# Kernel optimization log

Measured on AMD Instinct MI355X. Metric: run time of the kernel, lower is better.

Reference implementation:

```python
import jax, jax.numpy as jnp
import numpy as np


def setup_inputs() -> dict:
    key = jax.random.key(0)
    k1, k2, k3 = jax.random.split(key, 3)
    N, C, W = 32, 64, 4096
    F, WW = 128, 64
    x = jax.random.normal(k1, (N, C, W), dtype=jnp.float32)
    w = jax.random.normal(k2, (F, C, WW), dtype=jnp.float32)
    b = jax.random.normal(k3, (F,), dtype=jnp.float32)
    return {"x": x, "w": w, "b": b}


def reference(x, w, b):
    # FFT-based 1D cross-correlation (the original loops over N, F, C; here batched).
    # x: [N, C, W], w: [F, C, WW], b: [F]
    N, C, W = x.shape
    F, _, WW = w.shape
    pad = 0  # module's padding kwarg
    fftsize = 1 << int(np.ceil(np.log2(W + 2 * pad + WW - 1)))  # next_power2
    out_W = W + 2 * pad - WW + 1
    # rfft of zero-padded signals and filters
    xfft = jnp.fft.rfft(x, n=fftsize, axis=-1)          # [N, C, K]
    wfft = jnp.fft.rfft(w, n=fftsize, axis=-1)          # [F, C, K]
    # cross-correlation: multiply by conj of filter spectrum, sum over channels
    offt = jnp.einsum('nck,fck->nfk', xfft, jnp.conj(wfft))  # [N, F, K]
    out = jnp.fft.irfft(offt, n=fftsize, axis=-1)[..., :out_W]  # real part, first out_W samples
    return out + b[None, :, None]
```

## Files before the change

kernel.cpp:

```cpp
#include <hip/hip_runtime.h>


#define C_TOT   64
#define F_TOT   128
#define KW      64
#define OUT_W   4033
#define W_IN    4096
#define N_BATCH 32
#define T_BLK   256
#define XROW    4352
#define CH      2

typedef __attribute__((ext_vector_type(8))) short  short8;
typedef __attribute__((ext_vector_type(4))) float  floatx4;

union Frag { unsigned int u[4]; short8 v; };

__device__ inline unsigned short f32_to_bf16(float f) {
  unsigned int u = __float_as_uint(f);
  u += 0x7FFF + ((u >> 16) & 1);
  return (unsigned short)(u >> 16);
}

__device__ inline void async16(const unsigned short* g, unsigned short* l) {
  __builtin_amdgcn_global_load_lds(
      (const __attribute__((address_space(1))) unsigned int*)g,
      (__attribute__((address_space(3))) unsigned int*)l, 16, 0, 0);
}

__global__ __launch_bounds__(256) void conv1d_prep(
    const float* __restrict__ x, const float* __restrict__ w,
    unsigned short* __restrict__ xb, unsigned short* __restrict__ wsw) {
  int bid = blockIdx.x;
  if (bid < N_BATCH * C_TOT) {
    const float* src = x + (size_t)bid * W_IN;
    unsigned short* dst = xb + (size_t)bid * XROW;
    for (int i = threadIdx.x; i < XROW / 4; i += 256) {
      int t = i * 4;
      ushort4 o;
      if (t < W_IN) {
        float4 v = *(const float4*)(src + t);
        o.x = f32_to_bf16(v.x); o.y = f32_to_bf16(v.y);
        o.z = f32_to_bf16(v.z); o.w = f32_to_bf16(v.w);
      } else {
        o.x = o.y = o.z = o.w = 0;
      }
      *(ushort4*)(dst + t) = o;
    }
  } else {
    int i4 = (bid - N_BATCH * C_TOT) * 256 + threadIdx.x;
    if (i4 < F_TOT * C_TOT * KW / 4) {
      int k4 = (i4 & 15) * 4;
      int c  = (i4 >> 4) & 63;
      int f  = i4 >> 10;
      float4 v = *(const float4*)&w[(size_t)i4 * 4];
      ushort4 o;
      o.x = f32_to_bf16(v.x); o.y = f32_to_bf16(v.y);
      o.z = f32_to_bf16(v.z); o.w = f32_to_bf16(v.w);
      int chunk = (k4 >> 3) ^ (f & 7);
      *(ushort4*)&wsw[((size_t)(c * F_TOT + f) * 8 + chunk) * 8 + (k4 & 7)] = o;
    }
  }
}

__global__ __launch_bounds__(256, 2) void conv1d_mfma(
    const unsigned short* __restrict__ xb, const unsigned short* __restrict__ wsw,
    const float* __restrict__ b, float* __restrict__ out) {
  __shared__ union SM {
    unsigned short wls[2][CH * F_TOT * KW];
    float tr[32 * 256];
  } sm;

  const int tid  = threadIdx.x;
  const int lane = tid & 63;
  const int wv   = tid >> 6;
  const int q    = lane >> 4;
  const int col  = lane & 15;
  const int n    = blockIdx.y;
  const int t0   = blockIdx.x * T_BLK;
  const int fh2  = wv & 1;
  const int th   = wv >> 1;

  floatx4 acc[8][4];
#pragma unroll
  for (int ms = 0; ms < 8; ++ms)
#pragma unroll
    for (int ft = 0; ft < 4; ++ft) acc[ms][ft] = (floatx4)0.0f;

  const unsigned short* xrowb = xb + (size_t)(n * C_TOT) * XROW + t0
                              + 8 * col + 128 * th + 8 * q;

#define STAGE_W(cg, p)                                                          \
  {                                                                             \
    const unsigned short* wbase = wsw + (size_t)(cg) * (CH * F_TOT * KW);       \
    _Pragma("unroll")                                                           \
    for (int s = 0; s < 8; ++s) {                                               \
      int off = (wv * 8 + s) * 512;                                             \
      async16(wbase + off + lane * 8, &sm.wls[p][off]);                         \
    }                                                                           \
  }

  STAGE_W(0, 0)
  __syncthreads();

  for (int cg = 0; cg < C_TOT / CH; ++cg) {
    const int p = cg & 1;
    if (cg < C_TOT / CH - 1) STAGE_W(cg + 1, p ^ 1)

#pragma unroll
    for (int chl = 0; chl < CH; ++chl) {
      const unsigned short* xpb = xrowb + (size_t)(cg * CH + chl) * XROW;
      const unsigned short* wpb = &sm.wls[p][chl * F_TOT * KW];
#pragma unroll
      for (int h = 0; h < 2; ++h) {
        const uint4 d0 = *(const uint4*)(xpb + 32 * h);
        const uint4 d1 = *(const uint4*)(xpb + 32 * h + 8);
        const unsigned int D[8] = {d0.x, d0.y, d0.z, d0.w, d1.x, d1.y, d1.z, d1.w};
        Frag A[8];
#pragma unroll
        for (int s = 0; s < 4; ++s)
#pragma unroll
          for (int i = 0; i < 4; ++i) {
            A[2 * s].u[i]     = D[s + i];
            A[2 * s + 1].u[i] = (D[s + i] >> 16) | (D[s + i + 1] << 16);
          }
        const int bs = ((h * 4 + q) ^ (col & 7)) * 8;
#pragma unroll
        for (int ft = 0; ft < 4; ++ft) {
          const short8 bf =
              *(const short8*)&wpb[(fh2 * 64 + ft * 16 + col) * KW + bs];
#pragma unroll
          for (int ms = 0; ms < 8; ++ms)
            acc[ms][ft] =
                __builtin_amdgcn_mfma_f32_16x16x32_bf16(A[ms].v, bf, acc[ms][ft], 0, 0, 0);
        }
      }
    }
    __syncthreads();
  }

  const int fs_w  = fh2 * 16 + col;
  const int fs_r  = tid >> 3;
  const int seg   = tid & 7;
  const int f_r   = (fs_r >> 4) * 64 + (fs_r & 15);
  const size_t ob = ((size_t)n * F_TOT) * OUT_W;

#pragma unroll
  for (int j = 0; j < 4; ++j) {
#pragma unroll
    for (int r = 0; r < 4; ++r)
#pragma unroll
      for (int g = 0; g < 2; ++g) {
        float4 vv;
        vv.x = acc[g * 4 + 0][j][r];
        vv.y = acc[g * 4 + 1][j][r];
        vv.z = acc[g * 4 + 2][j][r];
        vv.w = acc[g * 4 + 3][j][r];
        int chunk = 8 * q + 2 * r + g + 32 * th;
        *(float4*)&sm.tr[fs_w * 256 + ((chunk ^ (fs_w & 7)) << 2)] = vv;
      }
    __syncthreads();
    const int f = f_r + 16 * j;
    const float bias = b[f];
    const size_t obf = ob + (size_t)f * OUT_W;
#pragma unroll
    for (int j2 = 0; j2 < 8; ++j2) {
      int chunk = seg + 8 * j2;
      float4 vv = *(const float4*)&sm.tr[fs_r * 256 + ((chunk ^ (fs_r & 7)) << 2)];
      vv.x += bias; vv.y += bias; vv.z += bias; vv.w += bias;
      int t = t0 + chunk * 4;
      if (t + 3 < OUT_W) {
        *(float4*)&out[obf + t] = vv;
      } else {
        float e[4] = {vv.x, vv.y, vv.z, vv.w};
#pragma unroll
        for (int u = 0; u < 4; ++u)
          if (t + u < OUT_W) out[obf + t + u] = e[u];
      }
    }
    __syncthreads();
  }
}

extern "C" void kernel_launch(void* const* d_in, const int* in_sizes, int n_in,
                              void* d_out, int out_size, void* d_ws, size_t ws_size,
                              hipStream_t stream) {
  const float* x = (const float*)d_in[0];
  const float* w = (const float*)d_in[1];
  const float* b = (const float*)d_in[2];
  float* out = (float*)d_out;

  unsigned short* wsw = (unsigned short*)d_ws;
  unsigned short* xb  = (unsigned short*)((char*)d_ws + (1 << 20));

  conv1d_prep<<<N_BATCH * C_TOT + 512, 256, 0, stream>>>(x, w, xb, wsw);

  dim3 grid((OUT_W + T_BLK - 1) / T_BLK, N_BATCH);
  conv1d_mfma<<<grid, 256, 0, stream>>>(xb, wsw, b, out);
}
```

Baseline: 196.8 us.

## Load filter fragments directly from global into registers with double-buffered prefetch

Drops the LDS staging of weights through async global-to-LDS copies and the per-channel-group barriers. Each wave now reads its B fragments straight from global or L2 into registers, using a plain [c][f][k] bf16 layout, and double-buffers both A and B registers across channels. This removes the LDS traffic and sync overhead from the main loop. In exchange each wave issues more global loads, weight reuse across waves in a block relies on cache, and register pressure rises, which could hurt occupancy at two blocks per CU.

Measured after the change: 254.8 us. 1.29x slower.

```diff
diff --git a/kernel.cpp b/kernel.cpp
--- a/kernel.cpp
+++ b/kernel.cpp
@@ -9,7 +9,6 @@
 #define N_BATCH 32
 #define T_BLK   256
 #define XROW    4352
-#define CH      2
 
 typedef __attribute__((ext_vector_type(8))) short  short8;
 typedef __attribute__((ext_vector_type(4))) float  floatx4;
@@ -22,15 +21,9 @@
   return (unsigned short)(u >> 16);
 }
 
-__device__ inline void async16(const unsigned short* g, unsigned short* l) {
-  __builtin_amdgcn_global_load_lds(
-      (const __attribute__((address_space(1))) unsigned int*)g,
-      (__attribute__((address_space(3))) unsigned int*)l, 16, 0, 0);
-}
-
 __global__ __launch_bounds__(256) void conv1d_prep(
     const float* __restrict__ x, const float* __restrict__ w,
-    unsigned short* __restrict__ xb, unsigned short* __restrict__ wsw) {
+    unsigned short* __restrict__ xb, unsigned short* __restrict__ wcf) {
   int bid = blockIdx.x;
   if (bid < N_BATCH * C_TOT) {
     const float* src = x + (size_t)bid * W_IN;
@@ -57,19 +50,15 @@
       ushort4 o;
       o.x = f32_to_bf16(v.x); o.y = f32_to_bf16(v.y);
       o.z = f32_to_bf16(v.z); o.w = f32_to_bf16(v.w);
-      int chunk = (k4 >> 3) ^ (f & 7);
-      *(ushort4*)&wsw[((size_t)(c * F_TOT + f) * 8 + chunk) * 8 + (k4 & 7)] = o;
+      *(ushort4*)&wcf[((size_t)c * F_TOT + f) * KW + k4] = o;
     }
   }
 }
 
 __global__ __launch_bounds__(256, 2) void conv1d_mfma(
-    const unsigned short* __restrict__ xb, const unsigned short* __restrict__ wsw,
+    const unsigned short* __restrict__ xb, const unsigned short* __restrict__ wcf,
     const float* __restrict__ b, float* __restrict__ out) {
-  __shared__ union SM {
-    unsigned short wls[2][CH * F_TOT * KW];
-    float tr[32 * 256];
-  } sm;
+  __shared__ float tr[32 * 256];
 
   const int tid  = threadIdx.x;
   const int lane = tid & 63;
@@ -89,54 +78,60 @@
 
   const unsigned short* xrowb = xb + (size_t)(n * C_TOT) * XROW + t0
                               + 8 * col + 128 * th + 8 * q;
+  const unsigned short* wB = wcf + (size_t)(fh2 * 64 + col) * KW + 8 * q;
 
-#define STAGE_W(cg, p)                                                          \
+#define LOADB(B, c)                                                             \
   {                                                                             \
-    const unsigned short* wbase = wsw + (size_t)(cg) * (CH * F_TOT * KW);       \
+    const unsigned short* wp = wB + (size_t)(c) * (F_TOT * KW);                 \
     _Pragma("unroll")                                                           \
-    for (int s = 0; s < 8; ++s) {                                               \
-      int off = (wv * 8 + s) * 512;                                             \
-      async16(wbase + off + lane * 8, &sm.wls[p][off]);                         \
+    for (int ft = 0; ft < 4; ++ft) {                                            \
+      B[0][ft] = *(const short8*)(wp + ft * 16 * KW);                           \
+      B[1][ft] = *(const short8*)(wp + ft * 16 * KW + 32);                      \
     }                                                                           \
   }
 
-  STAGE_W(0, 0)
-  __syncthreads();
+#define LOADA(A, c)                                                             \
+  {                                                                             \
+    const unsigned short* xp = xrowb + (size_t)(c) * XROW;                      \
+    A[0] = *(const uint4*)(xp);      A[1] = *(const uint4*)(xp + 8);            \
+    A[2] = *(const uint4*)(xp + 32); A[3] = *(const uint4*)(xp + 40);           \
+  }
 
-  for (int cg = 0; cg < C_TOT / CH; ++cg) {
-    const int p = cg & 1;
-    if (cg < C_TOT / CH - 1) STAGE_W(cg + 1, p ^ 1)
+#define COMPUTE(Ax, Bx)                                                         \
+  {                                                                             \
+    _Pragma("unroll")                                                           \
+    for (int h = 0; h < 2; ++h) {                                               \
+      const unsigned int D[8] = {Ax[2 * h].x, Ax[2 * h].y, Ax[2 * h].z,         \
+                                 Ax[2 * h].w, Ax[2 * h + 1].x, Ax[2 * h + 1].y, \
+                                 Ax[2 * h + 1].z, Ax[2 * h + 1].w};             \
+      Frag F8[8];                                                               \
+      _Pragma("unroll")                                                         \
+      for (int s = 0; s < 4; ++s)                                               \
+        _Pragma("unroll")                                                       \
+        for (int i = 0; i < 4; ++i) {                                           \
+          F8[2 * s].u[i]     = D[s + i];                                        \
+          F8[2 * s + 1].u[i] = (D[s + i] >> 16) | (D[s + i + 1] << 16);         \
+        }                                                                       \
+      _Pragma("unroll")                                                         \
+      for (int ft = 0; ft < 4; ++ft)                                            \
+        _Pragma("unroll")                                                       \
+        for (int ms = 0; ms < 8; ++ms)                                          \
+          acc[ms][ft] = __builtin_amdgcn_mfma_f32_16x16x32_bf16(                \
+              F8[ms].v, Bx[h][ft], acc[ms][ft], 0, 0, 0);                       \
+    }                                                                           \
+  }
 
-#pragma unroll
-    for (int chl = 0; chl < CH; ++chl) {
-      const unsigned short* xpb = xrowb + (size_t)(cg * CH + chl) * XROW;
-      const unsigned short* wpb = &sm.wls[p][chl * F_TOT * KW];
-#pragma unroll
-      for (int h = 0; h < 2; ++h) {
-        const uint4 d0 = *(const uint4*)(xpb + 32 * h);
-        const uint4 d1 = *(const uint4*)(xpb + 32 * h + 8);
-        const unsigned int D[8] = {d0.x, d0.y, d0.z, d0.w, d1.x, d1.y, d1.z, d1.w};
-        Frag A[8];
-#pragma unroll
-        for (int s = 0; s < 4; ++s)
-#pragma unroll
-          for (int i = 0; i < 4; ++i) {
-            A[2 * s].u[i]     = D[s + i];
-            A[2 * s + 1].u[i] = (D[s + i] >> 16) | (D[s + i + 1] << 16);
-          }
-        const int bs = ((h * 4 + q) ^ (col & 7)) * 8;
-#pragma unroll
-        for (int ft = 0; ft < 4; ++ft) {
-          const short8 bf =
-              *(const short8*)&wpb[(fh2 * 64 + ft * 16 + col) * KW + bs];
-#pragma unroll
-          for (int ms = 0; ms < 8; ++ms)
-            acc[ms][ft] =
-                __builtin_amdgcn_mfma_f32_16x16x32_bf16(A[ms].v, bf, acc[ms][ft], 0, 0, 0);
-        }
-      }
-    }
-    __syncthreads();
+  uint4  A0[4], A1[4];
+  short8 B0[2][4], B1[2][4];
+  LOADA(A0, 0)
+  LOADB(B0, 0)
+#pragma unroll 1
+  for (int c = 0; c < C_TOT; c += 2) {
+    LOADA(A1, c + 1)
+    LOADB(B1, c + 1)
+    COMPUTE(A0, B0)
+    if (c + 2 < C_TOT) { LOADA(A0, c + 2) LOADB(B0, c + 2) }
+    COMPUTE(A1, B1)
   }
 
   const int fs_w  = fh2 * 16 + col;
@@ -145,6 +140,7 @@
   const int f_r   = (fs_r >> 4) * 64 + (fs_r & 15);
   const size_t ob = ((size_t)n * F_TOT) * OUT_W;
 
+  __syncthreads();
 #pragma unroll
   for (int j = 0; j < 4; ++j) {
 #pragma unroll
@@ -157,7 +153,7 @@
         vv.z = acc[g * 4 + 2][j][r];
         vv.w = acc[g * 4 + 3][j][r];
         int chunk = 8 * q + 2 * r + g + 32 * th;
-        *(float4*)&sm.tr[fs_w * 256 + ((chunk ^ (fs_w & 7)) << 2)] = vv;
+        *(float4*)&tr[fs_w * 256 + ((chunk ^ (fs_w & 7)) << 2)] = vv;
       }
     __syncthreads();
     const int f = f_r + 16 * j;
@@ -166,7 +162,7 @@
 #pragma unroll
     for (int j2 = 0; j2 < 8; ++j2) {
       int chunk = seg + 8 * j2;
-      float4 vv = *(const float4*)&sm.tr[fs_r * 256 + ((chunk ^ (fs_r & 7)) << 2)];
+      float4 vv = *(const float4*)&tr[fs_r * 256 + ((chunk ^ (fs_r & 7)) << 2)];
       vv.x += bias; vv.y += bias; vv.z += bias; vv.w += bias;
       int t = t0 + chunk * 4;
       if (t + 3 < OUT_W) {
@@ -190,11 +186,11 @@
   const float* b = (const float*)d_in[2];
   float* out = (float*)d_out;
 
-  unsigned short* wsw = (unsigned short*)d_ws;
+  unsigned short* wcf = (unsigned short*)d_ws;
   unsigned short* xb  = (unsigned short*)((char*)d_ws + (1 << 20));
 
-  conv1d_prep<<<N_BATCH * C_TOT + 512, 256, 0, stream>>>(x, w, xb, wsw);
+  conv1d_prep<<<N_BATCH * C_TOT + 512, 256, 0, stream>>>(x, w, xb, wcf);
 
   dim3 grid((OUT_W + T_BLK - 1) / T_BLK, N_BATCH);
-  conv1d_mfma<<<grid, 256, 0, stream>>>(xb, wsw, b, out);
+  conv1d_mfma<<<grid, 256, 0, stream>>>(xb, wcf, b, out);
 }
```

## Fuse input bf16 conversion into conv kernel and split filters across grid z

Applied to the files above, without the earlier changes.

Drops the separate x-to-bf16 prep pass: the MFMA kernel now reads fp32 x directly and packs it to bf16 in registers, with clamped indices standing in for the old zero-padded rows. Filters are split into two halves over a new grid z dimension, which halves the accumulators and LDS weight buffer per block and raises the launch-bounds occupancy target to 3. This removes a full read-write pass over x, but each block now loads twice as many input bytes per MFMA, and x is reloaded by both filter halves.

Result: slower. 273.3 us (+38.9%).

```diff
diff --git a/kernel.cpp b/kernel.cpp
--- a/kernel.cpp
+++ b/kernel.cpp
@@ -1,4 +1,5 @@
 #include <hip/hip_runtime.h>
+#include <hip/hip_bf16.h>
 
 
 #define C_TOT   64
@@ -8,7 +9,6 @@
 #define W_IN    4096
 #define N_BATCH 32
 #define T_BLK   256
-#define XROW    4352
 #define CH      2
 
 typedef __attribute__((ext_vector_type(8))) short  short8;
@@ -22,6 +22,11 @@
   return (unsigned short)(u >> 16);
 }
 
+__device__ inline unsigned int pack2(float a, float bb) {
+  __hip_bfloat162 h = __float22bfloat162_rn(make_float2(a, bb));
+  return *(unsigned int*)&h;
+}
+
 __device__ inline void async16(const unsigned short* g, unsigned short* l) {
   __builtin_amdgcn_global_load_lds(
       (const __attribute__((address_space(1))) unsigned int*)g,
@@ -29,45 +34,27 @@
 }
 
 __global__ __launch_bounds__(256) void conv1d_prep(
-    const float* __restrict__ x, const float* __restrict__ w,
-    unsigned short* __restrict__ xb, unsigned short* __restrict__ wsw) {
-  int bid = blockIdx.x;
-  if (bid < N_BATCH * C_TOT) {
-    const float* src = x + (size_t)bid * W_IN;
-    unsigned short* dst = xb + (size_t)bid * XROW;
-    for (int i = threadIdx.x; i < XROW / 4; i += 256) {
-      int t = i * 4;
-      ushort4 o;
-      if (t < W_IN) {
-        float4 v = *(const float4*)(src + t);
-        o.x = f32_to_bf16(v.x); o.y = f32_to_bf16(v.y);
-        o.z = f32_to_bf16(v.z); o.w = f32_to_bf16(v.w);
-      } else {
-        o.x = o.y = o.z = o.w = 0;
-      }
-      *(ushort4*)(dst + t) = o;
-    }
-  } else {
-    int i4 = (bid - N_BATCH * C_TOT) * 256 + threadIdx.x;
-    if (i4 < F_TOT * C_TOT * KW / 4) {
-      int k4 = (i4 & 15) * 4;
-      int c  = (i4 >> 4) & 63;
-      int f  = i4 >> 10;
-      float4 v = *(const float4*)&w[(size_t)i4 * 4];
-      ushort4 o;
-      o.x = f32_to_bf16(v.x); o.y = f32_to_bf16(v.y);
-      o.z = f32_to_bf16(v.z); o.w = f32_to_bf16(v.w);
-      int chunk = (k4 >> 3) ^ (f & 7);
-      *(ushort4*)&wsw[((size_t)(c * F_TOT + f) * 8 + chunk) * 8 + (k4 & 7)] = o;
-    }
-  }
-}
-
-__global__ __launch_bounds__(256, 2) void conv1d_mfma(
-    const unsigned short* __restrict__ xb, const unsigned short* __restrict__ wsw,
+    const float* __restrict__ w, unsigned short* __restrict__ wsw) {
+  int i4 = blockIdx.x * 256 + threadIdx.x;
+  if (i4 < F_TOT * C_TOT * KW / 4) {
+    int k4 = (i4 & 15) * 4;
+    int c  = (i4 >> 4) & 63;
+    int f  = i4 >> 10;
+    float4 v = *(const float4*)&w[(size_t)i4 * 4];
+    ushort4 o;
+    o.x = f32_to_bf16(v.x); o.y = f32_to_bf16(v.y);
+    o.z = f32_to_bf16(v.z); o.w = f32_to_bf16(v.w);
+    int fh = f >> 6, fl = f & 63;
+    int chunk = (k4 >> 3) ^ (f & 7);
+    *(ushort4*)&wsw[((size_t)((c * 2 + fh) * 64 + fl)) * 64 + chunk * 8 + (k4 & 7)] = o;
+  }
+}
+
+__global__ __launch_bounds__(256, 3) void conv1d_mfma(
+    const float* __restrict__ x, const unsigned short* __restrict__ wsw,
     const float* __restrict__ b, float* __restrict__ out) {
   __shared__ union SM {
-    unsigned short wls[2][CH * F_TOT * KW];
+    unsigned short wls[2][CH * 64 * KW];
     float tr[32 * 256];
   } sm;
 
@@ -78,89 +65,103 @@
   const int col  = lane & 15;
   const int n    = blockIdx.y;
   const int t0   = blockIdx.x * T_BLK;
-  const int fh2  = wv & 1;
+  const int fh   = blockIdx.z;
   const int th   = wv >> 1;
-
-  floatx4 acc[8][4];
+  const int fq   = wv & 1;
+
+  floatx4 acc[8][2];
 #pragma unroll
   for (int ms = 0; ms < 8; ++ms)
 #pragma unroll
-    for (int ft = 0; ft < 4; ++ft) acc[ms][ft] = (floatx4)0.0f;
-
-  const unsigned short* xrowb = xb + (size_t)(n * C_TOT) * XROW + t0
-                              + 8 * col + 128 * th + 8 * q;
+    for (int ft = 0; ft < 2; ++ft) acc[ms][ft] = (floatx4)0.0f;
+
+  const int tb = t0 + 8 * col + 128 * th + 8 * q;
+  const float* xnb = x + (size_t)n * C_TOT * W_IN;
 
 #define STAGE_W(cg, p)                                                          \
   {                                                                             \
-    const unsigned short* wbase = wsw + (size_t)(cg) * (CH * F_TOT * KW);       \
     _Pragma("unroll")                                                           \
-    for (int s = 0; s < 8; ++s) {                                               \
-      int off = (wv * 8 + s) * 512;                                             \
-      async16(wbase + off + lane * 8, &sm.wls[p][off]);                         \
+    for (int s = 0; s < 4; ++s) {                                               \
+      int g   = s * 256 + tid;                                                  \
+      int chl = g >> 9;                                                         \
+      int wo  = (g & 511) * 8;                                                  \
+      async16(wsw + ((size_t)(((cg) * CH + chl) * 2 + fh)) * 4096 + wo,         \
+              &sm.wls[p][g * 8]);                                               \
+    }                                                                           \
+  }
+
+#define COMPUTE(p)                                                              \
+  {                                                                             \
+    _Pragma("unroll")                                                           \
+    for (int chl = 0; chl < CH; ++chl) {                                        \
+      const float* xr = xnb + (size_t)(cg * CH + chl) * W_IN;                   \
+      const unsigned short* wpb = &sm.wls[p][chl * 4096];                       \
+      _Pragma("unroll")                                                         \
+      for (int h = 0; h < 2; ++h) {                                             \
+        const int gt = tb + 32 * h;                                             \
+        float4 v0 = *(const float4*)(xr + min(gt,      W_IN - 4));              \
+        float4 v1 = *(const float4*)(xr + min(gt + 4,  W_IN - 4));              \
+        float4 v2 = *(const float4*)(xr + min(gt + 8,  W_IN - 4));              \
+        float4 v3 = *(const float4*)(xr + min(gt + 12, W_IN - 4));              \
+        const unsigned int D[8] = {                                             \
+            pack2(v0.x, v0.y), pack2(v0.z, v0.w),                               \
+            pack2(v1.x, v1.y), pack2(v1.z, v1.w),                               \
+            pack2(v2.x, v2.y), pack2(v2.z, v2.w),                               \
+            pack2(v3.x, v3.y), pack2(v3.z, v3.w)};                              \
+        Frag A[8];                                                              \
+        _Pragma("unroll")                                                       \
+        for (int s = 0; s < 4; ++s)                                             \
+          _Pragma("unroll")                                                     \
+          for (int i = 0; i < 4; ++i) {                                         \
+            A[2 * s].u[i]     = D[s + i];                                       \
+            A[2 * s + 1].u[i] = (D[s + i] >> 16) | (D[s + i + 1] << 16);        \
+          }                                                                     \
+        const int bs = ((h * 4 + q) ^ (col & 7)) * 8;                           \
+        _Pragma("unroll")                                                       \
+        for (int ft = 0; ft < 2; ++ft) {                                        \
+          const short8 bf =                                                     \
+              *(const short8*)&wpb[(fq * 32 + ft * 16 + col) * KW + bs];        \
+          _Pragma("unroll")                                                     \
+          for (int ms = 0; ms < 8; ++ms)                                        \
+            acc[ms][ft] = __builtin_amdgcn_mfma_f32_16x16x32_bf16(              \
+                A[ms].v, bf, acc[ms][ft], 0, 0, 0);                             \
+        }                                                                       \
+      }                                                                         \
     }                                                                           \
   }
 
   STAGE_W(0, 0)
   __syncthreads();
 
+#pragma unroll 1
   for (int cg = 0; cg < C_TOT / CH; ++cg) {
     const int p = cg & 1;
     if (cg < C_TOT / CH - 1) STAGE_W(cg + 1, p ^ 1)
-
-#pragma unroll
-    for (int chl = 0; chl < CH; ++chl) {
-      const unsigned short* xpb = xrowb + (size_t)(cg * CH + chl) * XROW;
-      const unsigned short* wpb = &sm.wls[p][chl * F_TOT * KW];
-#pragma unroll
-      for (int h = 0; h < 2; ++h) {
-        const uint4 d0 = *(const uint4*)(xpb + 32 * h);
-        const uint4 d1 = *(const uint4*)(xpb + 32 * h + 8);
-        const unsigned int D[8] = {d0.x, d0.y, d0.z, d0.w, d1.x, d1.y, d1.z, d1.w};
-        Frag A[8];
-#pragma unroll
-        for (int s = 0; s < 4; ++s)
-#pragma unroll
-          for (int i = 0; i < 4; ++i) {
-            A[2 * s].u[i]     = D[s + i];
-            A[2 * s + 1].u[i] = (D[s + i] >> 16) | (D[s + i + 1] << 16);
-          }
-        const int bs = ((h * 4 + q) ^ (col & 7)) * 8;
-#pragma unroll
-        for (int ft = 0; ft < 4; ++ft) {
-          const short8 bf =
-              *(const short8*)&wpb[(fh2 * 64 + ft * 16 + col) * KW + bs];
-#pragma unroll
-          for (int ms = 0; ms < 8; ++ms)
-            acc[ms][ft] =
-                __builtin_amdgcn_mfma_f32_16x16x32_bf16(A[ms].v, bf, acc[ms][ft], 0, 0, 0);
-        }
-      }
-    }
+    COMPUTE(p)
     __syncthreads();
   }
 
-  const int fs_w  = fh2 * 16 + col;
+  const int fs_w  = fq * 16 + col;
   const int fs_r  = tid >> 3;
   const int seg   = tid & 7;
-  const int f_r   = (fs_r >> 4) * 64 + (fs_r & 15);
   const size_t ob = ((size_t)n * F_TOT) * OUT_W;
 
 #pragma unroll
-  for (int j = 0; j < 4; ++j) {
+  for (int j = 0; j < 2; ++j) {
 #pragma unroll
     for (int r = 0; r < 4; ++r)
 #pragma unroll
-      for (int g = 0; g < 2; ++g) {
+      for (int g2 = 0; g2 < 2; ++g2) {
         float4 vv;
-        vv.x = acc[g * 4 + 0][j][r];
-        vv.y = acc[g * 4 + 1][j][r];
-        vv.z = acc[g * 4 + 2][j][r];
-        vv.w = acc[g * 4 + 3][j][r];
-        int chunk = 8 * q + 2 * r + g + 32 * th;
+        vv.x = acc[g2 * 4 + 0][j][r];
+        vv.y = acc[g2 * 4 + 1][j][r];
+        vv.z = acc[g2 * 4 + 2][j][r];
+        vv.w = acc[g2 * 4 + 3][j][r];
+        int chunk = 8 * q + 2 * r + g2 + 32 * th;
         *(float4*)&sm.tr[fs_w * 256 + ((chunk ^ (fs_w & 7)) << 2)] = vv;
       }
     __syncthreads();
-    const int f = f_r + 16 * j;
+    const int f = fh * 64 + (fs_r >> 4) * 32 + j * 16 + (fs_r & 15);
     const float bias = b[f];
     const size_t obf = ob + (size_t)f * OUT_W;
 #pragma unroll
@@ -191,10 +192,9 @@
   float* out = (float*)d_out;
 
   unsigned short* wsw = (unsigned short*)d_ws;
-  unsigned short* xb  = (unsigned short*)((char*)d_ws + (1 << 20));
-
-  conv1d_prep<<<N_BATCH * C_TOT + 512, 256, 0, stream>>>(x, w, xb, wsw);
-
-  dim3 grid((OUT_W + T_BLK - 1) / T_BLK, N_BATCH);
-  conv1d_mfma<<<grid, 256, 0, stream>>>(xb, wsw, b, out);
-}
+
+  conv1d_prep<<<(F_TOT * C_TOT * KW / 4 + 255) / 256, 256, 0, stream>>>(w, wsw);
+
+  dim3 grid((OUT_W + T_BLK - 1) / T_BLK, N_BATCH, 2);
+  conv1d_mfma<<<grid, 256, 0, stream>>>(x, wsw, b, out);
+}
```
